# Performance work log

Measured on AMD Instinct MI355X. Metric: run time of the kernel, lower is better.

Reference implementation:

```python
import jax, jax.numpy as jnp
import numpy as np
import math

INPUT_SIZE = 1024
B, L1, L2 = 8, 2048, 2048


def setup_inputs() -> dict:
    key = jax.random.key(0)
    ks = jax.random.split(key, 10)
    s = 1.0 / math.sqrt(INPUT_SIZE)
    return {
        "Q": jax.random.normal(ks[0], (B, L1, INPUT_SIZE), dtype=jnp.float32),
        "K": jax.random.normal(ks[1], (B, L2, INPUT_SIZE), dtype=jnp.float32),
        "V": jax.random.normal(ks[2], (B, L2, INPUT_SIZE), dtype=jnp.float32),
        "K_mask": jax.random.randint(ks[3], (B, L2), 0, 2, dtype=jnp.int32),
        "Wq": jax.random.normal(ks[4], (INPUT_SIZE, INPUT_SIZE), dtype=jnp.float32) * s,
        "bq": jax.random.normal(ks[5], (INPUT_SIZE,), dtype=jnp.float32) * s,
        "Wk": jax.random.normal(ks[6], (INPUT_SIZE, INPUT_SIZE), dtype=jnp.float32) * s,
        "bk": jax.random.normal(ks[7], (INPUT_SIZE,), dtype=jnp.float32) * s,
        "Wv": jax.random.normal(ks[8], (INPUT_SIZE, INPUT_SIZE), dtype=jnp.float32) * s,
        "bv": jax.random.normal(ks[9], (INPUT_SIZE,), dtype=jnp.float32) * s,
    }


def reference(Q, K, V, K_mask, Wq, bq, Wk, bk, Wv, bv):
    # Linear projections (torch Linear: x @ W.T + b)
    q = jnp.einsum('bld,ed->ble', Q, Wq) + bq
    k = jnp.einsum('bld,ed->ble', K, Wk) + bk
    v = jnp.einsum('bld,ed->ble', V, Wv) + bv
    # scores: [B, L1, L2], scaled by sqrt(input_size)
    scores = jnp.einsum('bqd,bkd->bqk', q, k) / math.sqrt(INPUT_SIZE)
    # K_mask == 1 marks padding -> -inf before softmax
    scores = jnp.where(K_mask[:, None, :] == 1, -jnp.inf, scores)
    alpha = jax.nn.softmax(scores, axis=-1)
    matched_seq = jnp.einsum('bqk,bkd->bqd', alpha, v)
    return matched_seq
```

## Files before the change

kernel.cpp:

```cpp
#include <hip/hip_runtime.h>


using u16 = unsigned short;
using frag_ab = __attribute__((ext_vector_type(8))) short;
using frag_cd = __attribute__((ext_vector_type(4))) float;

#define BAR() asm volatile("s_barrier" ::: "memory")
#define WAITV(n) asm volatile("s_waitcnt vmcnt(" #n ")" ::: "memory")
#define L(d, ab, h) (lds + (((d) * 4) + ((ab) * 2) + (h)) * 8192)

__device__ __forceinline__ u16 f2bf(float f) {
  union { float f; unsigned u; } c; c.f = f;
  unsigned u = c.u;
  return (u16)((u + 0x7FFFu + ((u >> 16) & 1u)) >> 16);
}
__device__ __forceinline__ u16 f2h(float f) {
  union { _Float16 h; u16 u; } c; c.h = (_Float16)f; return c.u;
}
__device__ __forceinline__ float h2f(u16 u) {
  union { u16 u; _Float16 h; } c; c.u = u; return (float)c.h;
}

__device__ __forceinline__ void async_ld16(const void* g, void* l) {
  __builtin_amdgcn_global_load_lds(
      (const __attribute__((address_space(1))) unsigned*)g,
      (__attribute__((address_space(3))) unsigned*)l, 16, 0, 0);
}

__global__ void cvt_f32_bf16(const float* __restrict__ in, u16* __restrict__ out, long n) {
  long i = ((long)blockIdx.x * 256 + threadIdx.x) * 4;
  if (i >= n) return;
  float4 v = *reinterpret_cast<const float4*>(in + i);
  *reinterpret_cast<ushort4*>(out + i) =
      make_ushort4(f2bf(v.x), f2bf(v.y), f2bf(v.z), f2bf(v.w));
}

__global__ void cvt3_f32_bf16(const float* __restrict__ q, const float* __restrict__ k,
                              const float* __restrict__ v, u16* __restrict__ out) {
  const float* in = blockIdx.z == 0 ? q : (blockIdx.z == 1 ? k : v);
  u16* o = out + (long)blockIdx.z * 16777216L;
  long i = ((long)blockIdx.x * 256 + threadIdx.x) * 4;
  float4 x = *reinterpret_cast<const float4*>(in + i);
  *reinterpret_cast<ushort4*>(o + i) =
      make_ushort4(f2bf(x.x), f2bf(x.y), f2bf(x.z), f2bf(x.w));
}

__device__ __forceinline__ void stage_half(const u16* __restrict__ g_rowbase,
                                           long Kstr, u16* l_half,
                                           int wave, int lane) {
  const int t = wave * 64 + lane;
  #pragma unroll
  for (int i = 0; i < 2; i++) {
    const int row = i * 64 + (t >> 3);
    const int cb  = (t & 7) * 16;
    const int cbs = cb ^ ((row & 7) << 4);
    async_ld16(g_rowbase + (long)row * Kstr + (cbs >> 1),
               l_half + i * 4096 + wave * 512);
  }
}

__device__ __forceinline__ frag_ab ld_frag(const u16* half_base, int r, int k) {
  const int idx = r * 64 + (k ^ ((r & 7) << 3));
  return *reinterpret_cast<const frag_ab*>(half_base + idx);
}

template<int OUT_MODE>
__device__ __forceinline__ void
gemm256_body(const u16* __restrict__ A, const u16* __restrict__ Bt,
             void* __restrict__ Cout, const float* __restrict__ bias,
             int M, int N, int K, long sA, long sB, long sC, float scale,
             u16* lds)
{
  const int gx = gridDim.x, gy = gridDim.y, gz = gridDim.z;
  const int nwg = gx * gy * gz;
  const int lin = ((int)blockIdx.z * gy + blockIdx.y) * gx + blockIdx.x;
  const int q8 = nwg >> 3, r8 = nwg & 7;
  const int xcd = lin & 7, idx8 = lin >> 3;
  const int swz = (xcd < r8 ? xcd * (q8 + 1) : r8 * (q8 + 1) + (xcd - r8) * q8) + idx8;
  const int z = swz / (gx * gy);
  const int rem = swz % (gx * gy);
  const int m0 = (rem / gx) * 256;
  const int n0 = (rem % gx) * 256;

  const u16* Ab = A + (long)z * sA;
  const u16* Bb = Bt + (long)z * sB;

  const int tid = threadIdx.x;
  const int wave = tid >> 6, lane = tid & 63;
  const int wm = wave >> 2;
  const int wn = wave & 3;
  const int ln15 = lane & 15, kof = (lane >> 4) * 8;
  const int rB0 = (wn & 1) * 64;
  const int NT = K >> 6;

  frag_cd acc[8][4];
  #pragma unroll
  for (int i = 0; i < 8; i++)
    #pragma unroll
    for (int j = 0; j < 4; j++)
      acc[i][j] = (frag_cd){0.f, 0.f, 0.f, 0.f};

  stage_half(Ab + (long)(m0 +   0) * K, K, L(0, 0, 0), wave, lane);
  stage_half(Ab + (long)(m0 + 128) * K, K, L(0, 0, 1), wave, lane);
  stage_half(Bb + (long)(n0 +   0) * K, K, L(0, 1, 0), wave, lane);
  stage_half(Bb + (long)(n0 + 128) * K, K, L(0, 1, 1), wave, lane);
  {
    const int t1 = (1 < NT) ? 1 : 0;
    stage_half(Bb + (long)(n0 +   0) * K + t1 * 64, K, L(1, 1, 0), wave, lane);
    stage_half(Bb + (long)(n0 + 128) * K + t1 * 64, K, L(1, 1, 1), wave, lane);
  }
  WAITV(4);
  BAR();

  for (int t = 0; t < NT; ++t) {
    const int d = t & 1;
    const u16* Al = L(d, 0, wm);
    const u16* Bl = L(d, 1, wn >> 1);
    const int tA = (t + 1 < NT) ? t + 1 : NT - 1;
    const int tB = (t + 2 < NT) ? t + 2 : NT - 1;

    frag_ab bf[4][2], af[2][2];

    #pragma unroll
    for (int bn = 0; bn < 4; ++bn)
      #pragma unroll
      for (int kk = 0; kk < 2; ++kk)
        bf[bn][kk] = ld_frag(Bl, rB0 + bn * 16 + ln15, kk * 32 + kof);
    #pragma unroll
    for (int am = 0; am < 2; ++am)
      #pragma unroll
      for (int kk = 0; kk < 2; ++kk)
        af[am][kk] = ld_frag(Al, am * 16 + ln15, kk * 32 + kof);
    stage_half(Ab + (long)(m0 +   0) * K + tA * 64, K, L(d ^ 1, 0, 0), wave, lane);
    stage_half(Ab + (long)(m0 + 128) * K + tA * 64, K, L(d ^ 1, 0, 1), wave, lane);
    BAR();
    __builtin_amdgcn_s_setprio(1);
    #pragma unroll
    for (int am = 0; am < 2; ++am)
      #pragma unroll
      for (int bn = 0; bn < 4; ++bn)
        #pragma unroll
        for (int kk = 0; kk < 2; ++kk)
          acc[am][bn] = __builtin_amdgcn_mfma_f32_16x16x32_bf16(af[am][kk], bf[bn][kk], acc[am][bn], 0, 0, 0);
    __builtin_amdgcn_s_setprio(0);
    BAR();

    #pragma unroll
    for (int am = 0; am < 2; ++am)
      #pragma unroll
      for (int kk = 0; kk < 2; ++kk)
        af[am][kk] = ld_frag(Al, (2 + am) * 16 + ln15, kk * 32 + kof);
    stage_half(Bb + (long)(n0 + 0) * K + tB * 64, K, L(d, 1, 0), wave, lane);
    BAR();
    __builtin_amdgcn_s_setprio(1);
    #pragma unroll
    for (int am = 0; am < 2; ++am)
      #pragma unroll
      for (int bn = 0; bn < 4; ++bn)
        #pragma unroll
        for (int kk = 0; kk < 2; ++kk)
          acc[2 + am][bn] = __builtin_amdgcn_mfma_f32_16x16x32_bf16(af[am][kk], bf[bn][kk], acc[2 + am][bn], 0, 0, 0);
    __builtin_amdgcn_s_setprio(0);
    BAR();

    #pragma unroll
    for (int am = 0; am < 2; ++am)
      #pragma unroll
      for (int kk = 0; kk < 2; ++kk)
        af[am][kk] = ld_frag(Al, (4 + am) * 16 + ln15, kk * 32 + kof);
    stage_half(Bb + (long)(n0 + 128) * K + tB * 64, K, L(d, 1, 1), wave, lane);
    BAR();
    __builtin_amdgcn_s_setprio(1);
    #pragma unroll
    for (int am = 0; am < 2; ++am)
      #pragma unroll
      for (int bn = 0; bn < 4; ++bn)
        #pragma unroll
        for (int kk = 0; kk < 2; ++kk)
          acc[4 + am][bn] = __builtin_amdgcn_mfma_f32_16x16x32_bf16(af[am][kk], bf[bn][kk], acc[4 + am][bn], 0, 0, 0);
    __builtin_amdgcn_s_setprio(0);
    BAR();

    #pragma unroll
    for (int am = 0; am < 2; ++am)
      #pragma unroll
      for (int kk = 0; kk < 2; ++kk)
        af[am][kk] = ld_frag(Al, (6 + am) * 16 + ln15, kk * 32 + kof);
    BAR();
    __builtin_amdgcn_s_setprio(1);
    #pragma unroll
    for (int am = 0; am < 2; ++am)
      #pragma unroll
      for (int bn = 0; bn < 4; ++bn)
        #pragma unroll
        for (int kk = 0; kk < 2; ++kk)
          acc[6 + am][bn] = __builtin_amdgcn_mfma_f32_16x16x32_bf16(af[am][kk], bf[bn][kk], acc[6 + am][bn], 0, 0, 0);
    __builtin_amdgcn_s_setprio(0);
    WAITV(4);
    BAR();
  }

  WAITV(0);
  BAR();

  const int cl = lane & 15;
  const int rb = (lane >> 4) * 4;
  #pragma unroll
  for (int bn = 0; bn < 4; ++bn) {
    const int gcol = n0 + wn * 64 + bn * 16 + cl;
    const float badd = bias ? bias[gcol] : 0.f;
    #pragma unroll
    for (int am = 0; am < 8; ++am) {
      #pragma unroll
      for (int r = 0; r < 4; ++r) {
        const int grow = m0 + wm * 128 + am * 16 + rb + r;
        const float val = acc[am][bn][r] * scale + badd;
        if (OUT_MODE == 0) {
          ((float*)Cout)[(long)z * sC + (long)grow * N + gcol] = val;
        } else if (OUT_MODE == 1) {
          ((u16*)Cout)[(long)z * sC + (long)grow * N + gcol] = f2bf(val);
        } else if (OUT_MODE == 3) {
          ((u16*)Cout)[(long)z * sC + (long)grow * N + gcol] = f2h(val);
        } else {
          const int bb = grow >> 11, l2 = grow & 2047;
          ((u16*)Cout)[((long)bb * N + gcol) * 2048 + l2] = f2bf(val);
        }
      }
    }
  }
}

__global__ void __launch_bounds__(512, 2)
proj_gemm(const u16* A, const u16* Bt, void* C, const float* bias,
          int M, int N, int K, long sA, long sB, long sC, float scale) {
  __shared__ u16 lds[8 * 8192];
  gemm256_body<1>(A, Bt, C, bias, M, N, K, sA, sB, sC, scale, lds);
}
__global__ void __launch_bounds__(512, 2)
projv_gemm(const u16* A, const u16* Bt, void* C, const float* bias,
           int M, int N, int K, long sA, long sB, long sC, float scale) {
  __shared__ u16 lds[8 * 8192];
  gemm256_body<2>(A, Bt, C, bias, M, N, K, sA, sB, sC, scale, lds);
}
__global__ void __launch_bounds__(512, 2)
qk_gemm(const u16* A, const u16* Bt, void* C, const float* bias,
        int M, int N, int K, long sA, long sB, long sC, float scale) {
  __shared__ u16 lds[8 * 8192];
  gemm256_body<3>(A, Bt, C, bias, M, N, K, sA, sB, sC, scale, lds);
}
__global__ void __launch_bounds__(512, 2)
pv_gemm(const u16* A, const u16* Bt, void* C, const float* bias,
        int M, int N, int K, long sA, long sB, long sC, float scale) {
  __shared__ u16 lds[8 * 8192];
  gemm256_body<0>(A, Bt, C, bias, M, N, K, sA, sB, sC, scale, lds);
}

__global__ void softmax_rows_h(const u16* __restrict__ S, const int* __restrict__ Km,
                               u16* __restrict__ P)
{
  const long row = blockIdx.x;
  const int b = (int)(row >> 11);
  const u16* s = S + row * 2048;
  const int* mask = Km + (long)b * 2048;
  u16* p = P + row * 2048;

  const int t = threadIdx.x;
  const int base = t * 8;

  ushort4 r0 = *reinterpret_cast<const ushort4*>(s + base);
  ushort4 r1 = *reinterpret_cast<const ushort4*>(s + base + 4);
  int4 mA = *reinterpret_cast<const int4*>(mask + base);
  int4 mB = *reinterpret_cast<const int4*>(mask + base + 4);

  float vals[8] = {h2f(r0.x), h2f(r0.y), h2f(r0.z), h2f(r0.w),
                   h2f(r1.x), h2f(r1.y), h2f(r1.z), h2f(r1.w)};
  const int mk[8] = {mA.x, mA.y, mA.z, mA.w, mB.x, mB.y, mB.z, mB.w};

  float mx = -3.0e38f;
  #pragma unroll
  for (int i = 0; i < 8; i++) if (!mk[i]) mx = fmaxf(mx, vals[i]);
  #pragma unroll
  for (int off = 32; off > 0; off >>= 1) mx = fmaxf(mx, __shfl_xor(mx, off));

  __shared__ float redm[4], reds[4];
  const int wave = t >> 6, lane = t & 63;
  if (lane == 0) redm[wave] = mx;
  __syncthreads();
  mx = fmaxf(fmaxf(redm[0], redm[1]), fmaxf(redm[2], redm[3]));

  float e[8]; float sum = 0.f;
  #pragma unroll
  for (int i = 0; i < 8; i++) { e[i] = mk[i] ? 0.f : __expf(vals[i] - mx); sum += e[i]; }
  #pragma unroll
  for (int off = 32; off > 0; off >>= 1) sum += __shfl_xor(sum, off);
  if (lane == 0) reds[wave] = sum;
  __syncthreads();
  sum = reds[0] + reds[1] + reds[2] + reds[3];
  const float inv = 1.f / sum;

  *reinterpret_cast<ushort4*>(p + base) =
      make_ushort4(f2bf(e[0]*inv), f2bf(e[1]*inv), f2bf(e[2]*inv), f2bf(e[3]*inv));
  *reinterpret_cast<ushort4*>(p + base + 4) =
      make_ushort4(f2bf(e[4]*inv), f2bf(e[5]*inv), f2bf(e[6]*inv), f2bf(e[7]*inv));
}

extern "C" void kernel_launch(void* const* d_in, const int* in_sizes, int n_in,
                              void* d_out, int out_size, void* d_ws, size_t ws_size,
                              hipStream_t stream) {
  (void)in_sizes; (void)n_in; (void)out_size;

  const float* Qin  = (const float*)d_in[0];
  const float* Kin  = (const float*)d_in[1];
  const float* Vin  = (const float*)d_in[2];
  const int*   Kmask = (const int*)d_in[3];
  const float* Wq = (const float*)d_in[4];
  const float* bq = (const float*)d_in[5];
  const float* Wk = (const float*)d_in[6];
  const float* bk = (const float*)d_in[7];
  const float* Wv = (const float*)d_in[8];
  const float* bv = (const float*)d_in[9];

  char* ws = (char*)d_ws;
  const size_t MB = 1024UL * 1024UL;
  const long NW = 1024L * 1024;
  const dim3 blk(256);
  const dim3 gblk(512);
  const float rs = 0.03125f;

  if (ws_size >= 226 * MB) {
    u16*  qb = (u16*)(ws);
    u16*  kb = (u16*)(ws + 32 * MB);
    u16*  vT = (u16*)(ws + 64 * MB);
    u16*  P  = (u16*)(ws + 96 * MB);
    u16*  Xq = (u16*)(ws + 96 * MB);
    u16*  S  = (u16*)(ws + 160 * MB);
    u16*  Wb = (u16*)(ws + 224 * MB);

    cvt3_f32_bf16<<<dim3(16384, 1, 3), blk, 0, stream>>>(Qin, Kin, Vin, Xq);

    cvt_f32_bf16<<<dim3(NW / 1024), blk, 0, stream>>>(Wq, Wb, NW);
    proj_gemm<<<dim3(4, 64, 1), gblk, 0, stream>>>(Xq, Wb, qb, bq,
        16384, 1024, 1024, 0, 0, 0, 1.f);

    cvt_f32_bf16<<<dim3(NW / 1024), blk, 0, stream>>>(Wk, Wb, NW);
    proj_gemm<<<dim3(4, 64, 1), gblk, 0, stream>>>(Xq + 16777216L, Wb, kb, bk,
        16384, 1024, 1024, 0, 0, 0, 1.f);

    cvt_f32_bf16<<<dim3(NW / 1024), blk, 0, stream>>>(Wv, Wb, NW);
    projv_gemm<<<dim3(4, 64, 1), gblk, 0, stream>>>(Xq + 2L * 16777216L, Wb, vT, bv,
        16384, 1024, 1024, 0, 0, 0, 1.f);

    qk_gemm<<<dim3(8, 8, 8), gblk, 0, stream>>>(qb, kb, S, nullptr,
        2048, 2048, 1024, 2048L * 1024, 2048L * 1024, 2048L * 2048, rs);
    softmax_rows_h<<<dim3(16384), blk, 0, stream>>>(S, Kmask, P);

    pv_gemm<<<dim3(4, 8, 8), gblk, 0, stream>>>(P, vT, d_out, nullptr,
        2048, 1024, 2048, 2048L * 2048, 1024L * 2048, 2048L * 1024, 1.f);
  } else if (ws_size >= 194 * MB) {
    u16*  qb = (u16*)(ws);
    u16*  kb = (u16*)(ws + 32 * MB);
    u16*  vT = (u16*)(ws + 64 * MB);
    u16*  P  = (u16*)(ws + 96 * MB);
    u16*  Xq = (u16*)(ws + 96 * MB);
    u16*  S  = (u16*)(ws + 160 * MB);
    u16*  Wb = (u16*)(ws + 192 * MB);

    cvt3_f32_bf16<<<dim3(16384, 1, 3), blk, 0, stream>>>(Qin, Kin, Vin, Xq);

    cvt_f32_bf16<<<dim3(NW / 1024), blk, 0, stream>>>(Wq, Wb, NW);
    proj_gemm<<<dim3(4, 64, 1), gblk, 0, stream>>>(Xq, Wb, qb, bq,
        16384, 1024, 1024, 0, 0, 0, 1.f);
    cvt_f32_bf16<<<dim3(NW / 1024), blk, 0, stream>>>(Wk, Wb, NW);
    proj_gemm<<<dim3(4, 64, 1), gblk, 0, stream>>>(Xq + 16777216L, Wb, kb, bk,
        16384, 1024, 1024, 0, 0, 0, 1.f);
    cvt_f32_bf16<<<dim3(NW / 1024), blk, 0, stream>>>(Wv, Wb, NW);
    projv_gemm<<<dim3(4, 64, 1), gblk, 0, stream>>>(Xq + 2L * 16777216L, Wb, vT, bv,
        16384, 1024, 1024, 0, 0, 0, 1.f);

    for (int h = 0; h < 2; h++) {
      const u16* qbH = qb + (long)(4 * h) * 2048 * 1024;
      const u16* kbH = kb + (long)(4 * h) * 2048 * 1024;
      qk_gemm<<<dim3(8, 8, 4), gblk, 0, stream>>>(qbH, kbH, S, nullptr,
          2048, 2048, 1024, 2048L * 1024, 2048L * 1024, 2048L * 2048, rs);
      softmax_rows_h<<<dim3(8192), blk, 0, stream>>>(
          S, Kmask + (long)(4 * h) * 2048, P + (long)(4 * h) * 2048 * 2048);
    }

    pv_gemm<<<dim3(4, 8, 8), gblk, 0, stream>>>(P, vT, d_out, nullptr,
        2048, 1024, 2048, 2048L * 2048, 1024L * 2048, 2048L * 1024, 1.f);
  } else {
    u16*  qb = (u16*)(ws);
    u16*  kb = (u16*)(ws + 32 * MB);
    u16*  vT = (u16*)(ws + 64 * MB);
    u16*  Xb = (u16*)(ws + 96 * MB);
    u16*  S  = (u16*)(ws + 96 * MB);
    u16*  P  = (u16*)(ws + 104 * MB);
    u16*  Wb = (u16*)(ws + 128 * MB);
    const long NQKV = 8L * 2048 * 1024;

    cvt_f32_bf16<<<dim3(NQKV / 1024), blk, 0, stream>>>(Qin, Xb, NQKV);
    cvt_f32_bf16<<<dim3(NW / 1024), blk, 0, stream>>>(Wq, Wb, NW);
    proj_gemm<<<dim3(4, 64, 1), gblk, 0, stream>>>(Xb, Wb, qb, bq,
        16384, 1024, 1024, 0, 0, 0, 1.f);
    cvt_f32_bf16<<<dim3(NQKV / 1024), blk, 0, stream>>>(Kin, Xb, NQKV);
    cvt_f32_bf16<<<dim3(NW / 1024), blk, 0, stream>>>(Wk, Wb, NW);
    proj_gemm<<<dim3(4, 64, 1), gblk, 0, stream>>>(Xb, Wb, kb, bk,
        16384, 1024, 1024, 0, 0, 0, 1.f);
    cvt_f32_bf16<<<dim3(NQKV / 1024), blk, 0, stream>>>(Vin, Xb, NQKV);
    cvt_f32_bf16<<<dim3(NW / 1024), blk, 0, stream>>>(Wv, Wb, NW);
    projv_gemm<<<dim3(4, 64, 1), gblk, 0, stream>>>(Xb, Wb, vT, bv,
        16384, 1024, 1024, 0, 0, 0, 1.f);

    for (int b = 0; b < 8; b++) {
      const u16* qbB = qb + (long)b * 2048 * 1024;
      const u16* kbB = kb + (long)b * 2048 * 1024;
      const u16* vTB = vT + (long)b * 1024 * 2048;
      float* outB = (float*)d_out + (long)b * 2048 * 1024;

      qk_gemm<<<dim3(8, 8, 1), gblk, 0, stream>>>(qbB, kbB, S, nullptr,
          2048, 2048, 1024, 0, 0, 0, rs);
      softmax_rows_h<<<dim3(2048), blk, 0, stream>>>(S, Kmask + (long)b * 2048, P);
      pv_gemm<<<dim3(4, 8, 1), gblk, 0, stream>>>(P, vTB, outB, nullptr,
          2048, 1024, 2048, 0, 0, 0, 1.f);
    }
  }
}
```

Measured before the change: 365.3 us.

## Fuse fp32-to-bf16 input conversion into a single batched QKV projection GEMM

Removes the separate activation conversion pass. The new projection kernel loads fp32 Q/K/V tiles straight from global memory into registers, packs them to bf16, and writes them into swizzled LDS while weight tiles stream asynchronously. All three projections run in one launch with z selecting the input, bias and output layout, and the three weight conversions are merged into one kernel. This avoids writing and re-reading about 96MB of bf16 activations plus several launches. In exchange it uses register-staged loads with occupancy 1 and more complex synchronization inside the main loop.

```diff
diff --git a/kernel.cpp b/kernel.cpp
--- a/kernel.cpp
+++ b/kernel.cpp
@@ -7,6 +7,8 @@
 
 #define BAR() asm volatile("s_barrier" ::: "memory")
 #define WAITV(n) asm volatile("s_waitcnt vmcnt(" #n ")" ::: "memory")
+#define WAITLGKM0() do { asm volatile("s_waitcnt lgkmcnt(0)" ::: "memory"); \
+                         __builtin_amdgcn_sched_barrier(0); } while (0)
 #define L(d, ab, h) (lds + (((d) * 4) + ((ab) * 2) + (h)) * 8192)
 
 __device__ __forceinline__ u16 f2bf(float f) {
@@ -20,6 +22,14 @@
 __device__ __forceinline__ float h2f(u16 u) {
   union { u16 u; _Float16 h; } c; c.u = u; return (float)c.h;
 }
+__device__ __forceinline__ frag_ab pack8(float4 x, float4 y) {
+  frag_ab p;
+  p[0] = (short)f2bf(x.x); p[1] = (short)f2bf(x.y);
+  p[2] = (short)f2bf(x.z); p[3] = (short)f2bf(x.w);
+  p[4] = (short)f2bf(y.x); p[5] = (short)f2bf(y.y);
+  p[6] = (short)f2bf(y.z); p[7] = (short)f2bf(y.w);
+  return p;
+}
 
 __device__ __forceinline__ void async_ld16(const void* g, void* l) {
   __builtin_amdgcn_global_load_lds(
@@ -27,22 +37,14 @@
       (__attribute__((address_space(3))) unsigned*)l, 16, 0, 0);
 }
 
-__global__ void cvt_f32_bf16(const float* __restrict__ in, u16* __restrict__ out, long n) {
+__global__ void cvtw3(const float* __restrict__ a, const float* __restrict__ b,
+                      const float* __restrict__ c, u16* __restrict__ out) {
+  const float* in = blockIdx.z == 0 ? a : (blockIdx.z == 1 ? b : c);
+  u16* o = out + (long)blockIdx.z * 1048576L;
   long i = ((long)blockIdx.x * 256 + threadIdx.x) * 4;
-  if (i >= n) return;
   float4 v = *reinterpret_cast<const float4*>(in + i);
-  *reinterpret_cast<ushort4*>(out + i) =
+  *reinterpret_cast<ushort4*>(o + i) =
       make_ushort4(f2bf(v.x), f2bf(v.y), f2bf(v.z), f2bf(v.w));
-}
-
-__global__ void cvt3_f32_bf16(const float* __restrict__ q, const float* __restrict__ k,
-                              const float* __restrict__ v, u16* __restrict__ out) {
-  const float* in = blockIdx.z == 0 ? q : (blockIdx.z == 1 ? k : v);
-  u16* o = out + (long)blockIdx.z * 16777216L;
-  long i = ((long)blockIdx.x * 256 + threadIdx.x) * 4;
-  float4 x = *reinterpret_cast<const float4*>(in + i);
-  *reinterpret_cast<ushort4*>(o + i) =
-      make_ushort4(f2bf(x.x), f2bf(x.y), f2bf(x.z), f2bf(x.w));
 }
 
 __device__ __forceinline__ void stage_half(const u16* __restrict__ g_rowbase,
@@ -63,13 +65,15 @@
   const int idx = r * 64 + (k ^ ((r & 7) << 3));
   return *reinterpret_cast<const frag_ab*>(half_base + idx);
 }
+__device__ __forceinline__ void st_frag(u16* half_base, int r, int s, frag_ab v) {
+  *reinterpret_cast<frag_ab*>(half_base + r * 64 + ((s ^ (r & 7)) << 3)) = v;
+}
 
 template<int OUT_MODE>
 __device__ __forceinline__ void
 gemm256_body(const u16* __restrict__ A, const u16* __restrict__ Bt,
-             void* __restrict__ Cout, const float* __restrict__ bias,
-             int M, int N, int K, long sA, long sB, long sC, float scale,
-             u16* lds)
+             void* __restrict__ Cout, int M, int N, int K,
+             long sA, long sB, long sC, float scale, u16* lds)
 {
   const int gx = gridDim.x, gy = gridDim.y, gz = gridDim.z;
   const int nwg = gx * gy * gz;
@@ -87,8 +91,7 @@
 
   const int tid = threadIdx.x;
   const int wave = tid >> 6, lane = tid & 63;
-  const int wm = wave >> 2;
-  const int wn = wave & 3;
+  const int wm = wave >> 2, wn = wave & 3;
   const int ln15 = lane & 15, kof = (lane >> 4) * 8;
   const int rB0 = (wn & 1) * 64;
   const int NT = K >> 6;
@@ -208,22 +211,16 @@
   #pragma unroll
   for (int bn = 0; bn < 4; ++bn) {
     const int gcol = n0 + wn * 64 + bn * 16 + cl;
-    const float badd = bias ? bias[gcol] : 0.f;
     #pragma unroll
     for (int am = 0; am < 8; ++am) {
       #pragma unroll
       for (int r = 0; r < 4; ++r) {
         const int grow = m0 + wm * 128 + am * 16 + rb + r;
-        const float val = acc[am][bn][r] * scale + badd;
+        const float val = acc[am][bn][r] * scale;
         if (OUT_MODE == 0) {
           ((float*)Cout)[(long)z * sC + (long)grow * N + gcol] = val;
-        } else if (OUT_MODE == 1) {
-          ((u16*)Cout)[(long)z * sC + (long)grow * N + gcol] = f2bf(val);
-        } else if (OUT_MODE == 3) {
+        } else {
           ((u16*)Cout)[(long)z * sC + (long)grow * N + gcol] = f2h(val);
-        } else {
-          const int bb = grow >> 11, l2 = grow & 2047;
-          ((u16*)Cout)[((long)bb * N + gcol) * 2048 + l2] = f2bf(val);
         }
       }
     }
@@ -231,28 +228,223 @@
 }
 
 __global__ void __launch_bounds__(512, 2)
-proj_gemm(const u16* A, const u16* Bt, void* C, const float* bias,
-          int M, int N, int K, long sA, long sB, long sC, float scale) {
-  __shared__ u16 lds[8 * 8192];
-  gemm256_body<1>(A, Bt, C, bias, M, N, K, sA, sB, sC, scale, lds);
-}
-__global__ void __launch_bounds__(512, 2)
-projv_gemm(const u16* A, const u16* Bt, void* C, const float* bias,
-           int M, int N, int K, long sA, long sB, long sC, float scale) {
-  __shared__ u16 lds[8 * 8192];
-  gemm256_body<2>(A, Bt, C, bias, M, N, K, sA, sB, sC, scale, lds);
-}
-__global__ void __launch_bounds__(512, 2)
-qk_gemm(const u16* A, const u16* Bt, void* C, const float* bias,
+qk_gemm(const u16* A, const u16* Bt, void* C,
         int M, int N, int K, long sA, long sB, long sC, float scale) {
   __shared__ u16 lds[8 * 8192];
-  gemm256_body<3>(A, Bt, C, bias, M, N, K, sA, sB, sC, scale, lds);
+  gemm256_body<3>(A, Bt, C, M, N, K, sA, sB, sC, scale, lds);
 }
 __global__ void __launch_bounds__(512, 2)
-pv_gemm(const u16* A, const u16* Bt, void* C, const float* bias,
+pv_gemm(const u16* A, const u16* Bt, void* C,
         int M, int N, int K, long sA, long sB, long sC, float scale) {
   __shared__ u16 lds[8 * 8192];
-  gemm256_body<0>(A, Bt, C, bias, M, N, K, sA, sB, sC, scale, lds);
+  gemm256_body<0>(A, Bt, C, M, N, K, sA, sB, sC, scale, lds);
+}
+
+
+#define FTILE(T, W, Ld) do {                                                   \
+    const int t = (T);                                                         \
+    const int d = t & 1;                                                       \
+    const u16* Al = L(d, 0, wm);                                               \
+    const u16* Bl = L(d, 1, wn >> 1);                                          \
+    const int tB = (t + 2 < 16) ? t + 2 : 15;                                  \
+    frag_ab bf[4][2], af[2][2];                                                \
+                  \
+    _Pragma("unroll")                                                          \
+    for (int bn = 0; bn < 4; ++bn)                                             \
+      _Pragma("unroll")                                                        \
+      for (int kk = 0; kk < 2; ++kk)                                           \
+        bf[bn][kk] = ld_frag(Bl, rB0 + bn * 16 + ln15, kk * 32 + kof);         \
+    _Pragma("unroll")                                                          \
+    for (int am = 0; am < 2; ++am)                                             \
+      _Pragma("unroll")                                                        \
+      for (int kk = 0; kk < 2; ++kk)                                           \
+        af[am][kk] = ld_frag(Al, am * 16 + ln15, kk * 32 + kof);               \
+    st_frag(L(d ^ 1, 0, 0), sr,      ss, pack8(W[0], W[1]));                   \
+    st_frag(L(d ^ 1, 0, 0), sr + 64, ss, pack8(W[2], W[3]));                   \
+    { const float* ap = Abf + (long)(m0 + sr) * 1024 + tB * 64 + ss * 8;       \
+      Ld[0] = *(const float4*)(ap);                                            \
+      Ld[1] = *(const float4*)(ap + 4);                                        \
+      Ld[2] = *(const float4*)(ap + 64L * 1024);                               \
+      Ld[3] = *(const float4*)(ap + 64L * 1024 + 4); }                         \
+    BAR();                                                                     \
+    __builtin_amdgcn_s_setprio(1);                                             \
+    _Pragma("unroll")                                                          \
+    for (int am = 0; am < 2; ++am)                                             \
+      _Pragma("unroll")                                                        \
+      for (int bn = 0; bn < 4; ++bn)                                           \
+        _Pragma("unroll")                                                      \
+        for (int kk = 0; kk < 2; ++kk)                                         \
+          acc[am][bn] = __builtin_amdgcn_mfma_f32_16x16x32_bf16(af[am][kk], bf[bn][kk], acc[am][bn], 0, 0, 0); \
+    __builtin_amdgcn_s_setprio(0);                                             \
+    BAR();                                                                     \
+         \
+    _Pragma("unroll")                                                          \
+    for (int am = 0; am < 2; ++am)                                             \
+      _Pragma("unroll")                                                        \
+      for (int kk = 0; kk < 2; ++kk)                                           \
+        af[am][kk] = ld_frag(Al, (2 + am) * 16 + ln15, kk * 32 + kof);         \
+    st_frag(L(d ^ 1, 0, 1), sr,      ss, pack8(W[4], W[5]));                   \
+    st_frag(L(d ^ 1, 0, 1), sr + 64, ss, pack8(W[6], W[7]));                   \
+    { const float* ap = Abf + (long)(m0 + 128 + sr) * 1024 + tB * 64 + ss * 8; \
+      Ld[4] = *(const float4*)(ap);                                            \
+      Ld[5] = *(const float4*)(ap + 4);                                        \
+      Ld[6] = *(const float4*)(ap + 64L * 1024);                               \
+      Ld[7] = *(const float4*)(ap + 64L * 1024 + 4); }                         \
+    stage_half(Wbz + (long)(n0 + 0) * 1024 + tB * 64, 1024, L(d, 1, 0), wave, lane); \
+    BAR();                                                                     \
+    __builtin_amdgcn_s_setprio(1);                                             \
+    _Pragma("unroll")                                                          \
+    for (int am = 0; am < 2; ++am)                                             \
+      _Pragma("unroll")                                                        \
+      for (int bn = 0; bn < 4; ++bn)                                           \
+        _Pragma("unroll")                                                      \
+        for (int kk = 0; kk < 2; ++kk)                                         \
+          acc[2 + am][bn] = __builtin_amdgcn_mfma_f32_16x16x32_bf16(af[am][kk], bf[bn][kk], acc[2 + am][bn], 0, 0, 0); \
+    __builtin_amdgcn_s_setprio(0);                                             \
+    BAR();                                                                     \
+                                \
+    _Pragma("unroll")                                                          \
+    for (int am = 0; am < 2; ++am)                                             \
+      _Pragma("unroll")                                                        \
+      for (int kk = 0; kk < 2; ++kk)                                           \
+        af[am][kk] = ld_frag(Al, (4 + am) * 16 + ln15, kk * 32 + kof);         \
+    stage_half(Wbz + (long)(n0 + 128) * 1024 + tB * 64, 1024, L(d, 1, 1), wave, lane); \
+    WAITLGKM0();                                                               \
+    BAR();                                                                     \
+    __builtin_amdgcn_s_setprio(1);                                             \
+    _Pragma("unroll")                                                          \
+    for (int am = 0; am < 2; ++am)                                             \
+      _Pragma("unroll")                                                        \
+      for (int bn = 0; bn < 4; ++bn)                                           \
+        _Pragma("unroll")                                                      \
+        for (int kk = 0; kk < 2; ++kk)                                         \
+          acc[4 + am][bn] = __builtin_amdgcn_mfma_f32_16x16x32_bf16(af[am][kk], bf[bn][kk], acc[4 + am][bn], 0, 0, 0); \
+    __builtin_amdgcn_s_setprio(0);                                             \
+    BAR();                                                                     \
+          \
+    _Pragma("unroll")                                                          \
+    for (int am = 0; am < 2; ++am)                                             \
+      _Pragma("unroll")                                                        \
+      for (int kk = 0; kk < 2; ++kk)                                           \
+        af[am][kk] = ld_frag(Al, (6 + am) * 16 + ln15, kk * 32 + kof);         \
+    BAR();                                                                     \
+    __builtin_amdgcn_s_setprio(1);                                             \
+    _Pragma("unroll")                                                          \
+    for (int am = 0; am < 2; ++am)                                             \
+      _Pragma("unroll")                                                        \
+      for (int bn = 0; bn < 4; ++bn)                                           \
+        _Pragma("unroll")                                                      \
+        for (int kk = 0; kk < 2; ++kk)                                         \
+          acc[6 + am][bn] = __builtin_amdgcn_mfma_f32_16x16x32_bf16(af[am][kk], bf[bn][kk], acc[6 + am][bn], 0, 0, 0); \
+    __builtin_amdgcn_s_setprio(0);                                             \
+    WAITV(12);                                                                 \
+    BAR();                                                                     \
+  } while (0)
+
+__global__ void __launch_bounds__(512, 1)
+proj3_gemm(const float* __restrict__ Qf, const float* __restrict__ Kf,
+           const float* __restrict__ Vf, const u16* __restrict__ Wb,
+           const float* __restrict__ bq, const float* __restrict__ bk,
+           const float* __restrict__ bv, u16* __restrict__ qkb,
+           u16* __restrict__ vT)
+{
+  __shared__ u16 lds[8 * 8192];
+
+  const int gx = gridDim.x, gy = gridDim.y;
+  const int nwg = gx * gy * gridDim.z;
+  const int lin = ((int)blockIdx.z * gy + blockIdx.y) * gx + blockIdx.x;
+  const int q8 = nwg >> 3, r8 = nwg & 7;
+  const int xcd = lin & 7, idx8 = lin >> 3;
+  const int swz = (xcd < r8 ? xcd * (q8 + 1) : r8 * (q8 + 1) + (xcd - r8) * q8) + idx8;
+  const int z = swz / (gx * gy);
+  const int rem = swz % (gx * gy);
+  const int m0 = (rem / gx) * 256;
+  const int n0 = (rem % gx) * 256;
+
+  const float* Abf = z == 0 ? Qf : (z == 1 ? Kf : Vf);
+  const u16* Wbz = Wb + (long)z * 1048576L;
+  const float* bias = z == 0 ? bq : (z == 1 ? bk : bv);
+
+  const int tid = threadIdx.x;
+  const int wave = tid >> 6, lane = tid & 63;
+  const int wm = wave >> 2, wn = wave & 3;
+  const int ln15 = lane & 15, kof = (lane >> 4) * 8;
+  const int rB0 = (wn & 1) * 64;
+  const int sr = tid >> 3;
+  const int ss = tid & 7;
+
+  frag_cd acc[8][4];
+  #pragma unroll
+  for (int i = 0; i < 8; i++)
+    #pragma unroll
+    for (int j = 0; j < 4; j++)
+      acc[i][j] = (frag_cd){0.f, 0.f, 0.f, 0.f};
+
+  float4 RA[8], RB[8];
+
+  {
+    const float* a0 = Abf + (long)(m0 + sr) * 1024 + ss * 8;
+    RA[0] = *(const float4*)(a0);
+    RA[1] = *(const float4*)(a0 + 4);
+    RA[2] = *(const float4*)(a0 +  64L * 1024);
+    RA[3] = *(const float4*)(a0 +  64L * 1024 + 4);
+    RA[4] = *(const float4*)(a0 + 128L * 1024);
+    RA[5] = *(const float4*)(a0 + 128L * 1024 + 4);
+    RA[6] = *(const float4*)(a0 + 192L * 1024);
+    RA[7] = *(const float4*)(a0 + 192L * 1024 + 4);
+  }
+  stage_half(Wbz + (long)(n0 +   0) * 1024, 1024, L(0, 1, 0), wave, lane);
+  stage_half(Wbz + (long)(n0 + 128) * 1024, 1024, L(0, 1, 1), wave, lane);
+  stage_half(Wbz + (long)(n0 +   0) * 1024 + 64, 1024, L(1, 1, 0), wave, lane);
+  stage_half(Wbz + (long)(n0 + 128) * 1024 + 64, 1024, L(1, 1, 1), wave, lane);
+  {
+    const float* a1 = Abf + (long)(m0 + sr) * 1024 + 64 + ss * 8;
+    RB[0] = *(const float4*)(a1);
+    RB[1] = *(const float4*)(a1 + 4);
+    RB[2] = *(const float4*)(a1 +  64L * 1024);
+    RB[3] = *(const float4*)(a1 +  64L * 1024 + 4);
+    RB[4] = *(const float4*)(a1 + 128L * 1024);
+    RB[5] = *(const float4*)(a1 + 128L * 1024 + 4);
+    RB[6] = *(const float4*)(a1 + 192L * 1024);
+    RB[7] = *(const float4*)(a1 + 192L * 1024 + 4);
+  }
+  WAITV(16);
+  st_frag(L(0, 0, 0), sr,      ss, pack8(RA[0], RA[1]));
+  st_frag(L(0, 0, 0), sr + 64, ss, pack8(RA[2], RA[3]));
+  st_frag(L(0, 0, 1), sr,      ss, pack8(RA[4], RA[5]));
+  st_frag(L(0, 0, 1), sr + 64, ss, pack8(RA[6], RA[7]));
+  WAITV(12);
+  WAITLGKM0();
+  BAR();
+
+  for (int t2 = 0; t2 < 16; t2 += 2) {
+    FTILE(t2,     RB, RA);
+    FTILE(t2 + 1, RA, RB);
+  }
+
+  WAITV(0);
+  BAR();
+
+  const int cl = lane & 15;
+  const int rb = (lane >> 4) * 4;
+  #pragma unroll
+  for (int bn = 0; bn < 4; ++bn) {
+    const int gcol = n0 + wn * 64 + bn * 16 + cl;
+    const float badd = bias[gcol];
+    #pragma unroll
+    for (int am = 0; am < 8; ++am) {
+      #pragma unroll
+      for (int r = 0; r < 4; ++r) {
+        const int grow = m0 + wm * 128 + am * 16 + rb + r;
+        const float val = acc[am][bn][r] + badd;
+        if (z < 2) {
+          qkb[(long)z * 16777216L + (long)grow * 1024 + gcol] = f2bf(val);
+        } else {
+          vT[((long)(grow >> 11) * 1024 + gcol) * 2048L + (grow & 2047)] = f2bf(val);
+        }
+      }
+    }
+  }
 }
 
 __global__ void softmax_rows_h(const u16* __restrict__ S, const int* __restrict__ Km,
@@ -322,105 +514,70 @@
 
   char* ws = (char*)d_ws;
   const size_t MB = 1024UL * 1024UL;
-  const long NW = 1024L * 1024;
   const dim3 blk(256);
   const dim3 gblk(512);
   const float rs = 0.03125f;
 
   if (ws_size >= 226 * MB) {
     u16*  qb = (u16*)(ws);
-    u16*  kb = (u16*)(ws + 32 * MB);
     u16*  vT = (u16*)(ws + 64 * MB);
+    u16*  Wb = (u16*)(ws + 96 * MB);
     u16*  P  = (u16*)(ws + 96 * MB);
-    u16*  Xq = (u16*)(ws + 96 * MB);
     u16*  S  = (u16*)(ws + 160 * MB);
-    u16*  Wb = (u16*)(ws + 224 * MB);
-
-    cvt3_f32_bf16<<<dim3(16384, 1, 3), blk, 0, stream>>>(Qin, Kin, Vin, Xq);
-
-    cvt_f32_bf16<<<dim3(NW / 1024), blk, 0, stream>>>(Wq, Wb, NW);
-    proj_gemm<<<dim3(4, 64, 1), gblk, 0, stream>>>(Xq, Wb, qb, bq,
-        16384, 1024, 1024, 0, 0, 0, 1.f);
-
-    cvt_f32_bf16<<<dim3(NW / 1024), blk, 0, stream>>>(Wk, Wb, NW);
-    proj_gemm<<<dim3(4, 64, 1), gblk, 0, stream>>>(Xq + 16777216L, Wb, kb, bk,
-        16384, 1024, 1024, 0, 0, 0, 1.f);
-
-    cvt_f32_bf16<<<dim3(NW / 1024), blk, 0, stream>>>(Wv, Wb, NW);
-    projv_gemm<<<dim3(4, 64, 1), gblk, 0, stream>>>(Xq + 2L * 16777216L, Wb, vT, bv,
-        16384, 1024, 1024, 0, 0, 0, 1.f);
-
-    qk_gemm<<<dim3(8, 8, 8), gblk, 0, stream>>>(qb, kb, S, nullptr,
+
+    cvtw3<<<dim3(1024, 1, 3), blk, 0, stream>>>(Wq, Wk, Wv, Wb);
+    proj3_gemm<<<dim3(4, 64, 3), gblk, 0, stream>>>(Qin, Kin, Vin, Wb,
+        bq, bk, bv, qb, vT);
+
+    qk_gemm<<<dim3(8, 8, 8), gblk, 0, stream>>>(qb, qb + 16777216L, S,
         2048, 2048, 1024, 2048L * 1024, 2048L * 1024, 2048L * 2048, rs);
     softmax_rows_h<<<dim3(16384), blk, 0, stream>>>(S, Kmask, P);
 
-    pv_gemm<<<dim3(4, 8, 8), gblk, 0, stream>>>(P, vT, d_out, nullptr,
+    pv_gemm<<<dim3(4, 8, 8), gblk, 0, stream>>>(P, vT, d_out,
         2048, 1024, 2048, 2048L * 2048, 1024L * 2048, 2048L * 1024, 1.f);
   } else if (ws_size >= 194 * MB) {
     u16*  qb = (u16*)(ws);
-    u16*  kb = (u16*)(ws + 32 * MB);
     u16*  vT = (u16*)(ws + 64 * MB);
+    u16*  Wb = (u16*)(ws + 96 * MB);
     u16*  P  = (u16*)(ws + 96 * MB);
-    u16*  Xq = (u16*)(ws + 96 * MB);
     u16*  S  = (u16*)(ws + 160 * MB);
-    u16*  Wb = (u16*)(ws + 192 * MB);
-
-    cvt3_f32_bf16<<<dim3(16384, 1, 3), blk, 0, stream>>>(Qin, Kin, Vin, Xq);
-
-    cvt_f32_bf16<<<dim3(NW / 1024), blk, 0, stream>>>(Wq, Wb, NW);
-    proj_gemm<<<dim3(4, 64, 1), gblk, 0, stream>>>(Xq, Wb, qb, bq,
-        16384, 1024, 1024, 0, 0, 0, 1.f);
-    cvt_f32_bf16<<<dim3(NW / 1024), blk, 0, stream>>>(Wk, Wb, NW);
-    proj_gemm<<<dim3(4, 64, 1), gblk, 0, stream>>>(Xq + 16777216L, Wb, kb, bk,
-        16384, 1024, 1024, 0, 0, 0, 1.f);
-    cvt_f32_bf16<<<dim3(NW / 1024), blk, 0, stream>>>(Wv, Wb, NW);
-    projv_gemm<<<dim3(4, 64, 1), gblk, 0, stream>>>(Xq + 2L * 16777216L, Wb, vT, bv,
-        16384, 1024, 1024, 0, 0, 0, 1.f);
+
+    cvtw3<<<dim3(1024, 1, 3), blk, 0, stream>>>(Wq, Wk, Wv, Wb);
+    proj3_gemm<<<dim3(4, 64, 3), gblk, 0, stream>>>(Qin, Kin, Vin, Wb,
+        bq, bk, bv, qb, vT);
 
     for (int h = 0; h < 2; h++) {
       const u16* qbH = qb + (long)(4 * h) * 2048 * 1024;
-      const u16* kbH = kb + (long)(4 * h) * 2048 * 1024;
-      qk_gemm<<<dim3(8, 8, 4), gblk, 0, stream>>>(qbH, kbH, S, nullptr,
+      const u16* kbH = qb + 16777216L + (long)(4 * h) * 2048 * 1024;
+      qk_gemm<<<dim3(8, 8, 4), gblk, 0, stream>>>(qbH, kbH, S,
           2048, 2048, 1024, 2048L * 1024, 2048L * 1024, 2048L * 2048, rs);
       softmax_rows_h<<<dim3(8192), blk, 0, stream>>>(
           S, Kmask + (long)(4 * h) * 2048, P + (long)(4 * h) * 2048 * 2048);
     }
 
-    pv_gemm<<<dim3(4, 8, 8), gblk, 0, stream>>>(P, vT, d_out, nullptr,
+    pv_gemm<<<dim3(4, 8, 8), gblk, 0, stream>>>(P, vT, d_out,
         2048, 1024, 2048, 2048L * 2048, 1024L * 2048, 2048L * 1024, 1.f);
   } else {
     u16*  qb = (u16*)(ws);
-    u16*  kb = (u16*)(ws + 32 * MB);
     u16*  vT = (u16*)(ws + 64 * MB);
-    u16*  Xb = (u16*)(ws + 96 * MB);
-    u16*  S  = (u16*)(ws + 96 * MB);
-    u16*  P  = (u16*)(ws + 104 * MB);
-    u16*  Wb = (u16*)(ws + 128 * MB);
-    const long NQKV = 8L * 2048 * 1024;
-
-    cvt_f32_bf16<<<dim3(NQKV / 1024), blk, 0, stream>>>(Qin, Xb, NQKV);
-    cvt_f32_bf16<<<dim3(NW / 1024), blk, 0, stream>>>(Wq, Wb, NW);
-    proj_gemm<<<dim3(4, 64, 1), gblk, 0, stream>>>(Xb, Wb, qb, bq,
-        16384, 1024, 1024, 0, 0, 0, 1.f);
-    cvt_f32_bf16<<<dim3(NQKV / 1024), blk, 0, stream>>>(Kin, Xb, NQKV);
-    cvt_f32_bf16<<<dim3(NW / 1024), blk, 0, stream>>>(Wk, Wb, NW);
-    proj_gemm<<<dim3(4, 64, 1), gblk, 0, stream>>>(Xb, Wb, kb, bk,
-        16384, 1024, 1024, 0, 0, 0, 1.f);
-    cvt_f32_bf16<<<dim3(NQKV / 1024), blk, 0, stream>>>(Vin, Xb, NQKV);
-    cvt_f32_bf16<<<dim3(NW / 1024), blk, 0, stream>>>(Wv, Wb, NW);
-    projv_gemm<<<dim3(4, 64, 1), gblk, 0, stream>>>(Xb, Wb, vT, bv,
-        16384, 1024, 1024, 0, 0, 0, 1.f);
+    u16*  Wb = (u16*)(ws + 96 * MB);
+    u16*  S  = (u16*)(ws + 104 * MB);
+    u16*  P  = (u16*)(ws + 112 * MB);
+
+    cvtw3<<<dim3(1024, 1, 3), blk, 0, stream>>>(Wq, Wk, Wv, Wb);
+    proj3_gemm<<<dim3(4, 64, 3), gblk, 0, stream>>>(Qin, Kin, Vin, Wb,
+        bq, bk, bv, qb, vT);
 
     for (int b = 0; b < 8; b++) {
       const u16* qbB = qb + (long)b * 2048 * 1024;
-      const u16* kbB = kb + (long)b * 2048 * 1024;
+      const u16* kbB = qb + 16777216L + (long)b * 2048 * 1024;
       const u16* vTB = vT + (long)b * 1024 * 2048;
       float* outB = (float*)d_out + (long)b * 2048 * 1024;
 
-      qk_gemm<<<dim3(8, 8, 1), gblk, 0, stream>>>(qbB, kbB, S, nullptr,
+      qk_gemm<<<dim3(8, 8, 1), gblk, 0, stream>>>(qbB, kbB, S,
           2048, 2048, 1024, 0, 0, 0, rs);
       softmax_rows_h<<<dim3(2048), blk, 0, stream>>>(S, Kmask + (long)b * 2048, P);
-      pv_gemm<<<dim3(4, 8, 1), gblk, 0, stream>>>(P, vTB, outB, nullptr,
+      pv_gemm<<<dim3(4, 8, 1), gblk, 0, stream>>>(P, vTB, outB,
           2048, 1024, 2048, 0, 0, 0, 1.f);
     }
   }
```

New measurement: 428.9 us. 17.4% more time.

## Stage GEMM epilogue through LDS for coalesced stores and batch weight conversions

Applied to the files above, without the earlier changes.

The GEMM epilogue now writes accumulators into a swizzled per-wave LDS tile and reads them back as 16-byte vectors, so global stores are row-contiguous instead of scattered 2- and 4-byte writes. The transposed-V path packs four consecutive rows into one ushort4 store. The three weight conversions are merged into one launch writing separate buffers, which removes two launches. This adds LDS round trips and waits in the epilogue and moves the weight buffer offset in the mid-size workspace path.

```diff
diff --git a/kernel.cpp b/kernel.cpp
--- a/kernel.cpp
+++ b/kernel.cpp
@@ -7,6 +7,8 @@
 
 #define BAR() asm volatile("s_barrier" ::: "memory")
 #define WAITV(n) asm volatile("s_waitcnt vmcnt(" #n ")" ::: "memory")
+#define WAITLGKM0() do { asm volatile("s_waitcnt lgkmcnt(0)" ::: "memory"); \
+                         __builtin_amdgcn_sched_barrier(0); } while (0)
 #define L(d, ab, h) (lds + (((d) * 4) + ((ab) * 2) + (h)) * 8192)
 
 __device__ __forceinline__ u16 f2bf(float f) {
@@ -27,11 +29,13 @@
       (__attribute__((address_space(3))) unsigned*)l, 16, 0, 0);
 }
 
-__global__ void cvt_f32_bf16(const float* __restrict__ in, u16* __restrict__ out, long n) {
+__global__ void cvtw3(const float* __restrict__ a, const float* __restrict__ b,
+                      const float* __restrict__ c, u16* __restrict__ out) {
+  const float* in = blockIdx.z == 0 ? a : (blockIdx.z == 1 ? b : c);
+  u16* o = out + (long)blockIdx.z * 1048576L;
   long i = ((long)blockIdx.x * 256 + threadIdx.x) * 4;
-  if (i >= n) return;
   float4 v = *reinterpret_cast<const float4*>(in + i);
-  *reinterpret_cast<ushort4*>(out + i) =
+  *reinterpret_cast<ushort4*>(o + i) =
       make_ushort4(f2bf(v.x), f2bf(v.y), f2bf(v.z), f2bf(v.w));
 }
 
@@ -87,8 +91,7 @@
 
   const int tid = threadIdx.x;
   const int wave = tid >> 6, lane = tid & 63;
-  const int wm = wave >> 2;
-  const int wn = wave & 3;
+  const int wm = wave >> 2, wn = wave & 3;
   const int ln15 = lane & 15, kof = (lane >> 4) * 8;
   const int rB0 = (wn & 1) * 64;
   const int NT = K >> 6;
@@ -205,26 +208,80 @@
 
   const int cl = lane & 15;
   const int rb = (lane >> 4) * 4;
-  #pragma unroll
-  for (int bn = 0; bn < 4; ++bn) {
-    const int gcol = n0 + wn * 64 + bn * 16 + cl;
-    const float badd = bias ? bias[gcol] : 0.f;
-    #pragma unroll
-    for (int am = 0; am < 8; ++am) {
-      #pragma unroll
-      for (int r = 0; r < 4; ++r) {
-        const int grow = m0 + wm * 128 + am * 16 + rb + r;
-        const float val = acc[am][bn][r] * scale + badd;
-        if (OUT_MODE == 0) {
-          ((float*)Cout)[(long)z * sC + (long)grow * N + gcol] = val;
-        } else if (OUT_MODE == 1) {
-          ((u16*)Cout)[(long)z * sC + (long)grow * N + gcol] = f2bf(val);
-        } else if (OUT_MODE == 3) {
-          ((u16*)Cout)[(long)z * sC + (long)grow * N + gcol] = f2h(val);
-        } else {
-          const int bb = grow >> 11, l2 = grow & 2047;
-          ((u16*)Cout)[((long)bb * N + gcol) * 2048 + l2] = f2bf(val);
+
+  if (OUT_MODE == 1 || OUT_MODE == 3) {
+    u16* Wt = lds + wave * 8192;
+    #pragma unroll
+    for (int am = 0; am < 8; ++am)
+      #pragma unroll
+      for (int bn = 0; bn < 4; ++bn) {
+        const int col = bn * 16 + cl;
+        const float badd = bias ? bias[n0 + wn * 64 + col] : 0.f;
+        #pragma unroll
+        for (int r = 0; r < 4; ++r) {
+          const int row = am * 16 + rb + r;
+          const int slot = (col >> 3) ^ ((row >> 2) & 7);
+          const float val = acc[am][bn][r] * scale + badd;
+          Wt[row * 64 + slot * 8 + (col & 7)] = (OUT_MODE == 1) ? f2bf(val) : f2h(val);
         }
+      }
+    WAITLGKM0();
+    u16* Cb = (u16*)Cout + (long)z * sC;
+    #pragma unroll
+    for (int i = 0; i < 16; ++i) {
+      const int row = (lane >> 3) + i * 8;
+      const int c = lane & 7;
+      const int slot = c ^ ((row >> 2) & 7);
+      frag_ab v = *reinterpret_cast<const frag_ab*>(Wt + row * 64 + slot * 8);
+      const long grow = m0 + wm * 128 + row;
+      const int gcol = n0 + wn * 64 + c * 8;
+      *reinterpret_cast<frag_ab*>(Cb + grow * N + gcol) = v;
+    }
+  } else if (OUT_MODE == 0) {
+    float* Wt = (float*)(void*)lds + wave * 4096;
+    float* Cb = (float*)Cout + (long)z * sC;
+    #pragma unroll
+    for (int p = 0; p < 2; ++p) {
+      #pragma unroll
+      for (int am = 0; am < 8; ++am)
+        #pragma unroll
+        for (int bn = 0; bn < 2; ++bn) {
+          const int col = bn * 16 + cl;
+          #pragma unroll
+          for (int r = 0; r < 4; ++r) {
+            const int row = am * 16 + rb + r;
+            const int slot = (col >> 2) ^ ((row >> 2) & 7);
+            Wt[row * 32 + slot * 4 + (col & 3)] = acc[am][2 * p + bn][r] * scale;
+          }
+        }
+      WAITLGKM0();
+      #pragma unroll
+      for (int i = 0; i < 16; ++i) {
+        const int row = (lane >> 3) + i * 8;
+        const int c = lane & 7;
+        const int slot = c ^ ((row >> 2) & 7);
+        float4 v = *reinterpret_cast<const float4*>(Wt + row * 32 + slot * 4);
+        const long grow = m0 + wm * 128 + row;
+        const int gcol = n0 + wn * 64 + p * 32 + c * 4;
+        *reinterpret_cast<float4*>(Cb + grow * N + gcol) = v;
+      }
+      if (p == 0) WAITLGKM0();
+    }
+  } else {
+    #pragma unroll
+    for (int bn = 0; bn < 4; ++bn) {
+      const int gcol = n0 + wn * 64 + bn * 16 + cl;
+      const float badd = bias ? bias[gcol] : 0.f;
+      #pragma unroll
+      for (int am = 0; am < 8; ++am) {
+        const int grow0 = m0 + wm * 128 + am * 16 + rb;
+        ushort4 pk;
+        pk.x = f2bf(acc[am][bn][0] * scale + badd);
+        pk.y = f2bf(acc[am][bn][1] * scale + badd);
+        pk.z = f2bf(acc[am][bn][2] * scale + badd);
+        pk.w = f2bf(acc[am][bn][3] * scale + badd);
+        const int bb = grow0 >> 11, l2 = grow0 & 2047;
+        *reinterpret_cast<ushort4*>((u16*)Cout + ((long)bb * N + gcol) * 2048L + l2) = pk;
       }
     }
   }
@@ -322,7 +379,6 @@
 
   char* ws = (char*)d_ws;
   const size_t MB = 1024UL * 1024UL;
-  const long NW = 1024L * 1024;
   const dim3 blk(256);
   const dim3 gblk(512);
   const float rs = 0.03125f;
@@ -337,17 +393,13 @@
     u16*  Wb = (u16*)(ws + 224 * MB);
 
     cvt3_f32_bf16<<<dim3(16384, 1, 3), blk, 0, stream>>>(Qin, Kin, Vin, Xq);
-
-    cvt_f32_bf16<<<dim3(NW / 1024), blk, 0, stream>>>(Wq, Wb, NW);
+    cvtw3<<<dim3(1024, 1, 3), blk, 0, stream>>>(Wq, Wk, Wv, Wb);
+
     proj_gemm<<<dim3(4, 64, 1), gblk, 0, stream>>>(Xq, Wb, qb, bq,
         16384, 1024, 1024, 0, 0, 0, 1.f);
-
-    cvt_f32_bf16<<<dim3(NW / 1024), blk, 0, stream>>>(Wk, Wb, NW);
-    proj_gemm<<<dim3(4, 64, 1), gblk, 0, stream>>>(Xq + 16777216L, Wb, kb, bk,
-        16384, 1024, 1024, 0, 0, 0, 1.f);
-
-    cvt_f32_bf16<<<dim3(NW / 1024), blk, 0, stream>>>(Wv, Wb, NW);
-    projv_gemm<<<dim3(4, 64, 1), gblk, 0, stream>>>(Xq + 2L * 16777216L, Wb, vT, bv,
+    proj_gemm<<<dim3(4, 64, 1), gblk, 0, stream>>>(Xq + 16777216L, Wb + 1048576L, kb, bk,
+        16384, 1024, 1024, 0, 0, 0, 1.f);
+    projv_gemm<<<dim3(4, 64, 1), gblk, 0, stream>>>(Xq + 2L * 16777216L, Wb + 2L * 1048576L, vT, bv,
         16384, 1024, 1024, 0, 0, 0, 1.f);
 
     qk_gemm<<<dim3(8, 8, 8), gblk, 0, stream>>>(qb, kb, S, nullptr,
@@ -363,18 +415,16 @@
     u16*  P  = (u16*)(ws + 96 * MB);
     u16*  Xq = (u16*)(ws + 96 * MB);
     u16*  S  = (u16*)(ws + 160 * MB);
-    u16*  Wb = (u16*)(ws + 192 * MB);
+    u16*  Wb = (u16*)(ws + 186 * MB);
 
     cvt3_f32_bf16<<<dim3(16384, 1, 3), blk, 0, stream>>>(Qin, Kin, Vin, Xq);
-
-    cvt_f32_bf16<<<dim3(NW / 1024), blk, 0, stream>>>(Wq, Wb, NW);
+    cvtw3<<<dim3(1024, 1, 3), blk, 0, stream>>>(Wq, Wk, Wv, Wb);
+
     proj_gemm<<<dim3(4, 64, 1), gblk, 0, stream>>>(Xq, Wb, qb, bq,
         16384, 1024, 1024, 0, 0, 0, 1.f);
-    cvt_f32_bf16<<<dim3(NW / 1024), blk, 0, stream>>>(Wk, Wb, NW);
-    proj_gemm<<<dim3(4, 64, 1), gblk, 0, stream>>>(Xq + 16777216L, Wb, kb, bk,
-        16384, 1024, 1024, 0, 0, 0, 1.f);
-    cvt_f32_bf16<<<dim3(NW / 1024), blk, 0, stream>>>(Wv, Wb, NW);
-    projv_gemm<<<dim3(4, 64, 1), gblk, 0, stream>>>(Xq + 2L * 16777216L, Wb, vT, bv,
+    proj_gemm<<<dim3(4, 64, 1), gblk, 0, stream>>>(Xq + 16777216L, Wb + 1048576L, kb, bk,
+        16384, 1024, 1024, 0, 0, 0, 1.f);
+    projv_gemm<<<dim3(4, 64, 1), gblk, 0, stream>>>(Xq + 2L * 16777216L, Wb + 2L * 1048576L, vT, bv,
         16384, 1024, 1024, 0, 0, 0, 1.f);
 
     for (int h = 0; h < 2; h++) {
@@ -397,19 +447,19 @@
     u16*  P  = (u16*)(ws + 104 * MB);
     u16*  Wb = (u16*)(ws + 128 * MB);
     const long NQKV = 8L * 2048 * 1024;
-
-    cvt_f32_bf16<<<dim3(NQKV / 1024), blk, 0, stream>>>(Qin, Xb, NQKV);
-    cvt_f32_bf16<<<dim3(NW / 1024), blk, 0, stream>>>(Wq, Wb, NW);
+    const long NW = 1024L * 1024;
+
+    cvtw3<<<dim3(1024, 1, 3), blk, 0, stream>>>(Wq, Wk, Wv, Wb);
+    cvt3_f32_bf16<<<dim3(16384, 1, 1), blk, 0, stream>>>(Qin, Qin, Qin, Xb);
     proj_gemm<<<dim3(4, 64, 1), gblk, 0, stream>>>(Xb, Wb, qb, bq,
         16384, 1024, 1024, 0, 0, 0, 1.f);
-    cvt_f32_bf16<<<dim3(NQKV / 1024), blk, 0, stream>>>(Kin, Xb, NQKV);
-    cvt_f32_bf16<<<dim3(NW / 1024), blk, 0, stream>>>(Wk, Wb, NW);
-    proj_gemm<<<dim3(4, 64, 1), gblk, 0, stream>>>(Xb, Wb, kb, bk,
-        16384, 1024, 1024, 0, 0, 0, 1.f);
-    cvt_f32_bf16<<<dim3(NQKV / 1024), blk, 0, stream>>>(Vin, Xb, NQKV);
-    cvt_f32_bf16<<<dim3(NW / 1024), blk, 0, stream>>>(Wv, Wb, NW);
-    projv_gemm<<<dim3(4, 64, 1), gblk, 0, stream>>>(Xb, Wb, vT, bv,
-        16384, 1024, 1024, 0, 0, 0, 1.f);
+    cvt3_f32_bf16<<<dim3(16384, 1, 1), blk, 0, stream>>>(Kin, Kin, Kin, Xb);
+    proj_gemm<<<dim3(4, 64, 1), gblk, 0, stream>>>(Xb, Wb + 1048576L, kb, bk,
+        16384, 1024, 1024, 0, 0, 0, 1.f);
+    cvt3_f32_bf16<<<dim3(16384, 1, 1), blk, 0, stream>>>(Vin, Vin, Vin, Xb);
+    projv_gemm<<<dim3(4, 64, 1), gblk, 0, stream>>>(Xb, Wb + 2L * 1048576L, vT, bv,
+        16384, 1024, 1024, 0, 0, 0, 1.f);
+    (void)NQKV; (void)NW;
 
     for (int b = 0; b < 8; b++) {
       const u16* qbB = qb + (long)b * 2048 * 1024;
```

Result: faster. 336.7 us (-7.8%).
